# Kernel optimization log

Hardware: AMD Instinct MI355X
Metric: run time of the kernel (lower is better)

Reference implementation:

```python
import jax, jax.numpy as jnp
import numpy as np

B, C, T = 128, 16, 2048
H = 256            # hidden_size
G = 4 * H          # gate dim (i, f, g, o in torch order)
NUM_OUT = 10


def setup_inputs() -> dict:
    key = jax.random.key(0)
    ks = jax.random.split(key, 7)
    s = 1.0 / np.sqrt(H)  # torch default LSTM init scale
    return {
        "x": jax.random.normal(ks[0], (B, C, T), dtype=jnp.float32),
        "w_ih": jax.random.uniform(ks[1], (G, C), minval=-s, maxval=s, dtype=jnp.float32),
        "w_hh": jax.random.uniform(ks[2], (G, H), minval=-s, maxval=s, dtype=jnp.float32),
        "b_ih": jax.random.uniform(ks[3], (G,), minval=-s, maxval=s, dtype=jnp.float32),
        "b_hh": jax.random.uniform(ks[4], (G,), minval=-s, maxval=s, dtype=jnp.float32),
        "w_out": jax.random.uniform(ks[5], (NUM_OUT, H), minval=-s, maxval=s, dtype=jnp.float32),
        "b_out": jax.random.uniform(ks[6], (NUM_OUT,), minval=-s, maxval=s, dtype=jnp.float32),
    }


def _lstm_last_hidden(x, w_ih, w_hh, b_ih, b_hh):
    # x: (B, C, T) -> (B, T, C)
    xt = jnp.swapaxes(x, 1, 2)
    # Precompute input projections for all timesteps: (B, T, 4H)
    xproj = jnp.einsum('btc,gc->btg', xt, w_ih) + b_ih + b_hh
    xs = jnp.swapaxes(xproj, 0, 1)  # (T, B, 4H) for scan

    h0 = jnp.zeros((xt.shape[0], w_hh.shape[1]), dtype=x.dtype)
    c0 = jnp.zeros_like(h0)

    def step(carry, xp):
        h, cell = carry
        gates = xp + h @ w_hh.T               # (B, 4H)
        i, f, g, o = jnp.split(gates, 4, axis=-1)  # torch gate order i,f,g,o
        i = jax.nn.sigmoid(i)
        f = jax.nn.sigmoid(f)
        g = jnp.tanh(g)
        o = jax.nn.sigmoid(o)
        cell = f * cell + i * g
        h = o * jnp.tanh(cell)
        return (h, cell), None

    (hT, _), _ = jax.lax.scan(step, (h0, c0), xs)
    return hT  # (B, H): hidden state at last timestep


def reference(x, w_ih, w_hh, b_ih, b_hh, w_out, b_out):
    # bn0 is Identity (c.normalize_data=True)
    hT = _lstm_last_hidden(x, w_ih, w_hh, b_ih, b_hh)
    logits = hT @ w_out.T + b_out  # (B, num_outputs)
    return jax.nn.log_softmax(logits, axis=1)
```

## Files before the change

### kernel.cpp

```cpp
#include <hip/hip_runtime.h>
#include <cstdint>
#include <cstddef>

#define NB 128
#define NC 16
#define NT 2048
#define NH 256
#define NG 1024
#define NO 10

typedef _Float16 f16;
typedef _Float16 h2 __attribute__((ext_vector_type(2)));
typedef _Float16 h8 __attribute__((ext_vector_type(8)));

#define HPHASE 544

static __device__ __forceinline__ float fdot2(h2 a, h2 b, float c) {
#if __has_builtin(__builtin_amdgcn_fdot2)
  return __builtin_amdgcn_fdot2(a, b, c, false);
#else
  return c + (float)a[0] * (float)b[0] + (float)a[1] * (float)b[1];
#endif
}

static __device__ __forceinline__ int sdot4(int a, int b, int c) {
#if __has_builtin(__builtin_amdgcn_sdot4)
  return __builtin_amdgcn_sdot4(a, b, c, false);
#else
  int r = c;
#pragma unroll
  for (int i = 0; i < 4; ++i)
    r += (int)(int8_t)(a >> (8 * i)) * (int)(int8_t)(b >> (8 * i));
  return r;
#endif
}

static __device__ __forceinline__ float pairswap(float v) {
  int r = __builtin_amdgcn_update_dpp(0, __builtin_bit_cast(int, v),
                                      0xB1, 0xF, 0xF, true);
  return __builtin_bit_cast(float, r);
}

static __device__ __forceinline__ float sigm(float x) {
  return __builtin_amdgcn_rcpf(1.f + __expf(-x));
}
static __device__ __forceinline__ float tanh_(float x) {
  return 1.f - 2.f * __builtin_amdgcn_rcpf(1.f + __expf(2.f * x));
}

__global__ void prepack_whh_i8(const float* __restrict__ whh,
                               int8_t* __restrict__ wq,
                               float* __restrict__ scale) {
  int row = blockIdx.x;
  int k   = threadIdx.x;
  float v = whh[row * NH + k];
  float m = fabsf(v);
  for (int off = 32; off; off >>= 1) m = fmaxf(m, __shfl_xor(m, off, 64));
  __shared__ float smax[4];
  if ((k & 63) == 0) smax[k >> 6] = m;
  __syncthreads();
  float mm = fmaxf(fmaxf(smax[0], smax[1]), fmaxf(smax[2], smax[3]));
  float s = fmaxf(mm, 1e-20f) / 127.f;
  int qv = (int)rintf(v / s);
  qv = min(127, max(-127, qv));
  wq[row * NH + k] = (int8_t)qv;
  if (k == 0) scale[row] = s;
}

__global__ __launch_bounds__(512, 1)
void lstm_main(const float* __restrict__ x,
               const float* __restrict__ w_ih,
               const float* __restrict__ b_ih,
               const float* __restrict__ b_hh,
               const float* __restrict__ w_out,
               const float* __restrict__ b_out,
               const int8_t* __restrict__ wq,
               const float* __restrict__ scales,
               float* __restrict__ out) {
  const int t = threadIdx.x;
  const int u = t >> 1;
  const int half = t & 1;
  const int b = blockIdx.x;

  __shared__ __align__(16) int8_t hq8[2 * HPHASE];
  __shared__ __align__(16) f16 xs[64][NC];
  __shared__ float hT[NH];
  __shared__ float lg[NO];

  int wi_[32], wf_[32], wg_[32], wo_[32];
  h2 wih[4][4];
  {
    const int4* pi = (const int4*)(wq + (size_t)u * NH + 128 * half);
    const int4* pf = (const int4*)(wq + (size_t)(256 + u) * NH + 128 * half);
    const int4* pg = (const int4*)(wq + (size_t)(512 + u) * NH + 128 * half);
    const int4* po = (const int4*)(wq + (size_t)(768 + u) * NH + 128 * half);
#pragma unroll
    for (int c = 0; c < 8; ++c) {
      int4 vi = pi[c], vf = pf[c], vg = pg[c], vo = po[c];
      wi_[4 * c + 0] = vi.x; wi_[4 * c + 1] = vi.y; wi_[4 * c + 2] = vi.z; wi_[4 * c + 3] = vi.w;
      wf_[4 * c + 0] = vf.x; wf_[4 * c + 1] = vf.y; wf_[4 * c + 2] = vf.z; wf_[4 * c + 3] = vf.w;
      wg_[4 * c + 0] = vg.x; wg_[4 * c + 1] = vg.y; wg_[4 * c + 2] = vg.z; wg_[4 * c + 3] = vg.w;
      wo_[4 * c + 0] = vo.x; wo_[4 * c + 1] = vo.y; wo_[4 * c + 2] = vo.z; wo_[4 * c + 3] = vo.w;
    }
  }
#pragma unroll
  for (int g4 = 0; g4 < 4; ++g4) {
    int row = u + 256 * g4;
#pragma unroll
    for (int uu = 0; uu < 4; ++uu) {
      h2 t2 = {(f16)w_ih[row * NC + 8 * half + 2 * uu],
               (f16)w_ih[row * NC + 8 * half + 2 * uu + 1]};
      wih[g4][uu] = t2;
    }
  }
  const float K = 1.f / 127.f;
  float sci = scales[u] * K;
  float scf = scales[256 + u] * K;
  float scg = scales[512 + u] * K;
  float sco = scales[768 + u] * K;
  float bi_ = half ? 0.f : b_ih[u] + b_hh[u];
  float bf_ = half ? 0.f : b_ih[256 + u] + b_hh[256 + u];
  float bg_ = half ? 0.f : b_ih[512 + u] + b_hh[512 + u];
  float bo_ = half ? 0.f : b_ih[768 + u] + b_hh[768 + u];

  for (int e = t; e < 2 * HPHASE; e += 512) hq8[e] = 0;
#pragma unroll
  for (int r = 0; r < 2; ++r) {
    int e = t + 512 * r;
    int cc = e >> 6, tt = e & 63;
    xs[tt][cc] = (f16)x[(size_t)(b * NC + cc) * NT + tt];
  }
  __syncthreads();

  float c_ = 0.f, h_last = 0.f;
  const int rdoff = 400 * half;
  const int wroff = 272 * half + u;

#pragma unroll 1
  for (int s = 0; s < NT; ++s) {
    const int p = s & 1;
    const int4* hrd = (const int4*)(hq8 + p * HPHASE + rdoff);

    float fi = bi_, ff = bf_, fg_ = bg_, fo = bo_;
    {
      h8 xv = *(const h8*)&xs[s & 63][8 * half];
#pragma unroll
      for (int uu = 0; uu < 4; ++uu) {
        h2 xp = {xv[2 * uu], xv[2 * uu + 1]};
        fi = fdot2(xp, wih[0][uu], fi);
        ff = fdot2(xp, wih[1][uu], ff);
        fg_ = fdot2(xp, wih[2][uu], fg_);
        fo = fdot2(xp, wih[3][uu], fo);
      }
    }

    int ai = 0, af = 0, ag = 0, ao = 0;
#pragma unroll
    for (int c = 0; c < 8; ++c) {
      int4 hv = hrd[c];
      ai = sdot4(hv.x, wi_[4 * c + 0], ai); ai = sdot4(hv.y, wi_[4 * c + 1], ai);
      ai = sdot4(hv.z, wi_[4 * c + 2], ai); ai = sdot4(hv.w, wi_[4 * c + 3], ai);
      af = sdot4(hv.x, wf_[4 * c + 0], af); af = sdot4(hv.y, wf_[4 * c + 1], af);
      af = sdot4(hv.z, wf_[4 * c + 2], af); af = sdot4(hv.w, wf_[4 * c + 3], af);
      ag = sdot4(hv.x, wg_[4 * c + 0], ag); ag = sdot4(hv.y, wg_[4 * c + 1], ag);
      ag = sdot4(hv.z, wg_[4 * c + 2], ag); ag = sdot4(hv.w, wg_[4 * c + 3], ag);
      ao = sdot4(hv.x, wo_[4 * c + 0], ao); ao = sdot4(hv.y, wo_[4 * c + 1], ao);
      ao = sdot4(hv.z, wo_[4 * c + 2], ao); ao = sdot4(hv.w, wo_[4 * c + 3], ao);
    }

    float vi = fi + (float)ai * sci;
    float vf = ff + (float)af * scf;
    float vg = fg_ + (float)ag * scg;
    float vo = fo + (float)ao * sco;
    vi += pairswap(vi); vf += pairswap(vf); vg += pairswap(vg); vo += pairswap(vo);

    float ig = sigm(vi);
    float fgate = sigm(vf);
    float gv = tanh_(vg);
    float og = sigm(vo);
    c_ = fgate * c_ + ig * gv;
    float hh = og * tanh_(c_);
    h_last = hh;
    hq8[(1 - p) * HPHASE + wroff] = (int8_t)(int)rintf(hh * 127.f);

    if ((s & 63) == 63 && s != NT - 1) {
      __syncthreads();
#pragma unroll
      for (int r = 0; r < 2; ++r) {
        int e = t + 512 * r;
        int cc = e >> 6, tt = e & 63;
        xs[tt][cc] = (f16)x[(size_t)(b * NC + cc) * NT + (s + 1) + tt];
      }
    }
    __syncthreads();
  }

  if (!half) hT[u] = h_last;
  __syncthreads();
  if (t < NO) {
    float acc = b_out[t];
    for (int k = 0; k < NH; ++k) acc += hT[k] * w_out[t * NH + k];
    lg[t] = acc;
  }
  __syncthreads();
  if (t == 0) {
    float m = lg[0];
    for (int o = 1; o < NO; ++o) m = fmaxf(m, lg[o]);
    float ssum = 0.f;
    for (int o = 0; o < NO; ++o) ssum += __expf(lg[o] - m);
    float lse = m + __logf(ssum);
    for (int o = 0; o < NO; ++o) out[b * NO + o] = lg[o] - lse;
  }
}

extern "C" void kernel_launch(void* const* d_in, const int* in_sizes, int n_in,
                              void* d_out, int out_size, void* d_ws, size_t ws_size,
                              hipStream_t stream) {
  const float* x    = (const float*)d_in[0];
  const float* wih  = (const float*)d_in[1];
  const float* whh  = (const float*)d_in[2];
  const float* bih  = (const float*)d_in[3];
  const float* bhh  = (const float*)d_in[4];
  const float* wout = (const float*)d_in[5];
  const float* bout = (const float*)d_in[6];
  float* out = (float*)d_out;
  int8_t* wq = (int8_t*)d_ws;
  float* scales = (float*)((char*)d_ws + NG * NH);

  hipLaunchKernelGGL(prepack_whh_i8, dim3(NG), dim3(NH), 0, stream, whh, wq, scales);
  hipLaunchKernelGGL(lstm_main, dim3(NB), dim3(512), 0, stream,
                     x, wih, bih, bhh, wout, bout, wq, scales, out);
}
```

Measured before the change: 1.819 ms.

## Compute recurrent int8 matvec with MFMA instead of per-thread sdot4

Replaces the per-thread sdot4 recurrent dot products with i8 MFMA 16x16x32 ops. Each wave holds a 128-row slice of the quantized W_hh in registers, and h is broadcast as the A operand. Gate pre-activations go to a shared buffer and are read back after an extra barrier each step. Most of the MFMA work is wasted because only one row of the A tile carries real data, and the extra __syncthreads per step lengthens the serial critical path.

```diff
diff --git a/kernel.cpp b/kernel.cpp
--- a/kernel.cpp
+++ b/kernel.cpp
@@ -12,26 +12,13 @@
 typedef _Float16 f16;
 typedef _Float16 h2 __attribute__((ext_vector_type(2)));
 typedef _Float16 h8 __attribute__((ext_vector_type(8)));
-
-#define HPHASE 544
+typedef int i32x4 __attribute__((ext_vector_type(4)));
 
 static __device__ __forceinline__ float fdot2(h2 a, h2 b, float c) {
 #if __has_builtin(__builtin_amdgcn_fdot2)
   return __builtin_amdgcn_fdot2(a, b, c, false);
 #else
   return c + (float)a[0] * (float)b[0] + (float)a[1] * (float)b[1];
-#endif
-}
-
-static __device__ __forceinline__ int sdot4(int a, int b, int c) {
-#if __has_builtin(__builtin_amdgcn_sdot4)
-  return __builtin_amdgcn_sdot4(a, b, c, false);
-#else
-  int r = c;
-#pragma unroll
-  for (int i = 0; i < 4; ++i)
-    r += (int)(int8_t)(a >> (8 * i)) * (int)(int8_t)(b >> (8 * i));
-  return r;
 #endif
 }
 
@@ -67,7 +54,7 @@
   if (k == 0) scale[row] = s;
 }
 
-__global__ __launch_bounds__(512, 1)
+__global__ __launch_bounds__(512, 2)
 void lstm_main(const float* __restrict__ x,
                const float* __restrict__ w_ih,
                const float* __restrict__ b_ih,
@@ -78,31 +65,32 @@
                const float* __restrict__ scales,
                float* __restrict__ out) {
   const int t = threadIdx.x;
+  const int l = t & 63;
+  const int w = t >> 6;
   const int u = t >> 1;
   const int half = t & 1;
   const int b = blockIdx.x;
 
-  __shared__ __align__(16) int8_t hq8[2 * HPHASE];
+  __shared__ __align__(16) int8_t hq[2][NH];
+  __shared__ int gbuf[NG];
   __shared__ __align__(16) f16 xs[64][NC];
   __shared__ float hT[NH];
   __shared__ float lg[NO];
 
-  int wi_[32], wf_[32], wg_[32], wo_[32];
+  long bw[8][8];
+  {
+    const int row16 = l & 15;
+    const int koff = (l >> 4) * 8;
+#pragma unroll
+    for (int nt = 0; nt < 8; ++nt) {
+      const int g0 = (w * 8 + nt) * 16;
+      const int8_t* rp = wq + (size_t)(g0 + row16) * NH + koff;
+#pragma unroll
+      for (int kt = 0; kt < 8; ++kt)
+        bw[nt][kt] = *(const long*)(rp + kt * 32);
+    }
+  }
   h2 wih[4][4];
-  {
-    const int4* pi = (const int4*)(wq + (size_t)u * NH + 128 * half);
-    const int4* pf = (const int4*)(wq + (size_t)(256 + u) * NH + 128 * half);
-    const int4* pg = (const int4*)(wq + (size_t)(512 + u) * NH + 128 * half);
-    const int4* po = (const int4*)(wq + (size_t)(768 + u) * NH + 128 * half);
-#pragma unroll
-    for (int c = 0; c < 8; ++c) {
-      int4 vi = pi[c], vf = pf[c], vg = pg[c], vo = po[c];
-      wi_[4 * c + 0] = vi.x; wi_[4 * c + 1] = vi.y; wi_[4 * c + 2] = vi.z; wi_[4 * c + 3] = vi.w;
-      wf_[4 * c + 0] = vf.x; wf_[4 * c + 1] = vf.y; wf_[4 * c + 2] = vf.z; wf_[4 * c + 3] = vf.w;
-      wg_[4 * c + 0] = vg.x; wg_[4 * c + 1] = vg.y; wg_[4 * c + 2] = vg.z; wg_[4 * c + 3] = vg.w;
-      wo_[4 * c + 0] = vo.x; wo_[4 * c + 1] = vo.y; wo_[4 * c + 2] = vo.z; wo_[4 * c + 3] = vo.w;
-    }
-  }
 #pragma unroll
   for (int g4 = 0; g4 < 4; ++g4) {
     int row = u + 256 * g4;
@@ -114,16 +102,16 @@
     }
   }
   const float K = 1.f / 127.f;
-  float sci = scales[u] * K;
-  float scf = scales[256 + u] * K;
-  float scg = scales[512 + u] * K;
-  float sco = scales[768 + u] * K;
+  float sci = half ? 0.f : scales[u] * K;
+  float scf = half ? 0.f : scales[256 + u] * K;
+  float scg = half ? 0.f : scales[512 + u] * K;
+  float sco = half ? 0.f : scales[768 + u] * K;
   float bi_ = half ? 0.f : b_ih[u] + b_hh[u];
   float bf_ = half ? 0.f : b_ih[256 + u] + b_hh[256 + u];
   float bg_ = half ? 0.f : b_ih[512 + u] + b_hh[512 + u];
   float bo_ = half ? 0.f : b_ih[768 + u] + b_hh[768 + u];
 
-  for (int e = t; e < 2 * HPHASE; e += 512) hq8[e] = 0;
+  ((int8_t*)hq)[t] = 0;
 #pragma unroll
   for (int r = 0; r < 2; ++r) {
     int e = t + 512 * r;
@@ -133,13 +121,29 @@
   __syncthreads();
 
   float c_ = 0.f, h_last = 0.f;
-  const int rdoff = 400 * half;
-  const int wroff = 272 * half + u;
+  const int agrp = (l >> 4) * 8;
 
 #pragma unroll 1
   for (int s = 0; s < NT; ++s) {
     const int p = s & 1;
-    const int4* hrd = (const int4*)(hq8 + p * HPHASE + rdoff);
+
+    long a_[8];
+    {
+      const int8_t* hp = hq[p] + agrp;
+#pragma unroll
+      for (int kt = 0; kt < 8; ++kt)
+        a_[kt] = *(const long*)(hp + kt * 32);
+    }
+#pragma unroll
+    for (int nt = 0; nt < 8; ++nt) {
+      i32x4 acc = {0, 0, 0, 0};
+#pragma unroll
+      for (int kt = 0; kt < 8; ++kt)
+        acc = __builtin_amdgcn_mfma_i32_16x16x32_i8(a_[kt], bw[nt][kt], acc,
+                                                    0, 0, 0);
+      if (l < 16) gbuf[(w * 8 + nt) * 16 + l] = acc[0];
+    }
+    __syncthreads();
 
     float fi = bi_, ff = bf_, fg_ = bg_, fo = bo_;
     {
@@ -153,25 +157,10 @@
         fo = fdot2(xp, wih[3][uu], fo);
       }
     }
-
-    int ai = 0, af = 0, ag = 0, ao = 0;
-#pragma unroll
-    for (int c = 0; c < 8; ++c) {
-      int4 hv = hrd[c];
-      ai = sdot4(hv.x, wi_[4 * c + 0], ai); ai = sdot4(hv.y, wi_[4 * c + 1], ai);
-      ai = sdot4(hv.z, wi_[4 * c + 2], ai); ai = sdot4(hv.w, wi_[4 * c + 3], ai);
-      af = sdot4(hv.x, wf_[4 * c + 0], af); af = sdot4(hv.y, wf_[4 * c + 1], af);
-      af = sdot4(hv.z, wf_[4 * c + 2], af); af = sdot4(hv.w, wf_[4 * c + 3], af);
-      ag = sdot4(hv.x, wg_[4 * c + 0], ag); ag = sdot4(hv.y, wg_[4 * c + 1], ag);
-      ag = sdot4(hv.z, wg_[4 * c + 2], ag); ag = sdot4(hv.w, wg_[4 * c + 3], ag);
-      ao = sdot4(hv.x, wo_[4 * c + 0], ao); ao = sdot4(hv.y, wo_[4 * c + 1], ao);
-      ao = sdot4(hv.z, wo_[4 * c + 2], ao); ao = sdot4(hv.w, wo_[4 * c + 3], ao);
-    }
-
-    float vi = fi + (float)ai * sci;
-    float vf = ff + (float)af * scf;
-    float vg = fg_ + (float)ag * scg;
-    float vo = fo + (float)ao * sco;
+    float vi = fi + (float)gbuf[u] * sci;
+    float vf = ff + (float)gbuf[256 + u] * scf;
+    float vg = fg_ + (float)gbuf[512 + u] * scg;
+    float vo = fo + (float)gbuf[768 + u] * sco;
     vi += pairswap(vi); vf += pairswap(vf); vg += pairswap(vg); vo += pairswap(vo);
 
     float ig = sigm(vi);
@@ -181,7 +170,7 @@
     c_ = fgate * c_ + ig * gv;
     float hh = og * tanh_(c_);
     h_last = hh;
-    hq8[(1 - p) * HPHASE + wroff] = (int8_t)(int)rintf(hh * 127.f);
+    if (!half) hq[1 - p][u] = (int8_t)(int)rintf(hh * 127.f);
 
     if ((s & 63) == 63 && s != NT - 1) {
       __syncthreads();
```

Result: slower. 3.039 ms (+67.1%).
